# Performance work log

Hardware: AMD Instinct MI355X
Metric: run time of the kernel (lower is better)

The kernel has to match this reference:

```python
import math
import jax, jax.numpy as jnp
import numpy as np

B, N, C = 2, 2048, 1024
H = 16
D = C // H  # 64
LN_EPS = 1e-5


def setup_inputs() -> dict:
    key = jax.random.key(0)
    ks = jax.random.split(key, 5)
    x = jax.random.normal(ks[0], (B, N, C), dtype=jnp.float32)
    w_qkv = jax.random.normal(ks[1], (C, 3 * C), dtype=jnp.float32) * 0.02
    w_proj = jax.random.normal(ks[2], (C, C), dtype=jnp.float32) * 0.02
    b_proj = jnp.zeros((C,), dtype=jnp.float32)
    ln_w = jnp.ones((D,), dtype=jnp.float32) + jax.random.normal(ks[3], (D,), dtype=jnp.float32) * 0.02
    ln_b = jax.random.normal(ks[4], (D,), dtype=jnp.float32) * 0.02
    return {"x": x, "w_qkv": w_qkv, "w_proj": w_proj, "b_proj": b_proj,
            "ln_w": ln_w, "ln_b": ln_b}


def _layernorm(t, w, b):
    mu = jnp.mean(t, axis=-1, keepdims=True)
    var = jnp.var(t, axis=-1, keepdims=True)
    return (t - mu) * jax.lax.rsqrt(var + LN_EPS) * w + b


def reference(x, w_qkv, w_proj, b_proj, ln_w, ln_b):
    b, n, c = x.shape
    h, d = H, c // H
    # QKV projection (no bias): [b,n,3c] -> [3,b,h,n,d]
    qkv = (x @ w_qkv).reshape(b, n, 3, h, d).transpose(2, 0, 3, 1, 4)
    q, k, v = qkv[0], qkv[1], qkv[2]
    # per-head LayerNorm on q and k (qk_norm)
    q = _layernorm(q, ln_w, ln_b)
    k = _layernorm(k, ln_w, ln_b)
    # NOTE: source multiplies q by sqrt(head_dim) (faithful to original)
    q = q * jnp.asarray(math.sqrt(d), dtype=q.dtype)
    scores = jnp.einsum('bhnd,bhmd->bhnm', q, k)  # [b,h,n,n]
    mask_value = -jnp.finfo(scores.dtype).max
    causal = jnp.tril(jnp.ones((n, n), dtype=bool))
    scores = jnp.where(causal, scores, mask_value)
    attn = jax.nn.softmax(scores, axis=-1)
    out = jnp.einsum('bhnm,bhmd->bhnd', attn, v)  # [b,h,n,d]
    out = out.transpose(0, 2, 1, 3).reshape(b, n, c)  # b n (h d)
    return out @ w_proj + b_proj
```

## Files before the change

### kernel.cpp

```cpp
#include <hip/hip_runtime.h>

#define LOG2E 1.4426950408889634f

typedef _Float16 f16x8_t __attribute__((ext_vector_type(8)));
typedef _Float16 f16x4_t __attribute__((ext_vector_type(4)));
typedef _Float16 f16x2_t __attribute__((ext_vector_type(2)));
typedef float    f32x4_t __attribute__((ext_vector_type(4)));

#define MFMA32(a, b, c) __builtin_amdgcn_mfma_f32_16x16x32_f16(a, b, c, 0, 0, 0)
#define MFMA16(a, b, c) __builtin_amdgcn_mfma_f32_16x16x16f16(a, b, c, 0, 0, 0)

__device__ __forceinline__ void async_copy16(void* lds, const void* g) {
    __builtin_amdgcn_global_load_lds(
        (const __attribute__((address_space(1))) unsigned char*)g,
        (__attribute__((address_space(3))) unsigned char*)lds, 16, 0, 0);
}

__global__ void cast_f32_f16_k(const float* __restrict__ in, _Float16* __restrict__ out, int n4) {
    int i = blockIdx.x * blockDim.x + threadIdx.x;
    if (i >= n4) return;
    float4 v = ((const float4*)in)[i];
    f16x4_t o = { (_Float16)v.x, (_Float16)v.y, (_Float16)v.z, (_Float16)v.w };
    ((f16x4_t*)out)[i] = o;
}

__global__ void transpose_cast_k(const float* __restrict__ in, _Float16* __restrict__ out,
                                 int R, int C) {
    __shared__ _Float16 tl[64][65];
    const int t = threadIdx.x;
    const int c = t & 63;
    const int r4 = t >> 6;
    const int r0 = blockIdx.y * 64, c0 = blockIdx.x * 64;
#pragma unroll
    for (int i = 0; i < 16; ++i) {
        int r = r4 + i * 4;
        tl[c][r] = (_Float16)in[(size_t)(r0 + r) * C + c0 + c];
    }
    __syncthreads();
#pragma unroll
    for (int i = 0; i < 16; ++i) {
        int rr = r4 + i * 4;
        out[(size_t)(c0 + rr) * R + r0 + c] = tl[rr][c];
    }
}

__global__ void vtrans_k(const _Float16* __restrict__ qkv, _Float16* __restrict__ VTg) {
    __shared__ _Float16 tl[64][68];
    const int tid = threadIdx.x;
    const int bh = blockIdx.x;
    const int b = bh >> 4, h = bh & 15;
    const int t = blockIdx.y;
    const int c = tid & 63;
    const int r4 = tid >> 6;
#pragma unroll
    for (int i = 0; i < 16; ++i) {
        int r = r4 + i * 4;
        tl[c][r] = qkv[(size_t)(b * 2048 + t * 64 + r) * 3072 + 2048 + h * 64 + c];
    }
    __syncthreads();
    const size_t obase = (size_t)bh * 131072 + (size_t)t * 4096;
#pragma unroll
    for (int e = 0; e < 2; ++e) {
        const int ci = tid * 2 + e;
        const int d = ci >> 3, w = ci & 7;
        const int pq = w ^ (d & 7);
        const int base = (pq >> 2) * 32 + (pq & 3) * 4;
        f16x4_t v0 = *(const f16x4_t*)&tl[d][base];
        f16x4_t v1 = *(const f16x4_t*)&tl[d][base + 16];
        f16x8_t val = __builtin_shufflevector(v0, v1, 0, 1, 2, 3, 4, 5, 6, 7);
        *(f16x8_t*)&VTg[obase + ci * 8] = val;
    }
}

template <typename OutT, bool BIAS>
__global__ __launch_bounds__(256, 3)
void gemm_f16_k(const _Float16* __restrict__ A, const _Float16* __restrict__ BT,
                OutT* __restrict__ C, const float* __restrict__ bias,
                int M, int N, int K) {
    __shared__ _Float16 As[2][128][32];
    __shared__ _Float16 Bs[2][128][32];
    const int tid = threadIdx.x;
    const int wid = tid >> 6, lane = tid & 63;
    const int qd = lane >> 4, ln = lane & 15;
    const int m0 = blockIdx.x * 128, n0 = blockIdx.y * 128;
    const int wm = (wid >> 1) * 64, wn = (wid & 1) * 64;

    f32x4_t acc[4][4] = {};

    const int srow = lane >> 2;
    const int skk  = (lane & 3) * 8;

    for (int k0 = 0; k0 < K; k0 += 64) {
        __syncthreads();
#pragma unroll
        for (int p = 0; p < 4; ++p) {
            const int seg = p * 4 + wid;
            const int s   = seg >> 3;
            const int rg  = seg & 7;
            const int row = rg * 16 + srow;
            const size_t goff = (size_t)row * K + k0 + s * 32 + skk;
            async_copy16(&As[0][0][0] + seg * 512, A  + (size_t)m0 * K + goff);
            async_copy16(&Bs[0][0][0] + seg * 512, BT + (size_t)n0 * K + goff);
        }
        __syncthreads();
#pragma unroll
        for (int s = 0; s < 2; ++s) {
            f16x8_t a[4], b[4];
#pragma unroll
            for (int i = 0; i < 4; ++i)
                a[i] = *(const f16x8_t*)&As[s][wm + i * 16 + ln][qd * 8];
#pragma unroll
            for (int j = 0; j < 4; ++j)
                b[j] = *(const f16x8_t*)&Bs[s][wn + j * 16 + ln][qd * 8];
#pragma unroll
            for (int i = 0; i < 4; ++i)
#pragma unroll
                for (int j = 0; j < 4; ++j)
                    acc[i][j] = MFMA32(a[i], b[j], acc[i][j]);
        }
    }
#pragma unroll
    for (int i = 0; i < 4; ++i)
#pragma unroll
        for (int j = 0; j < 4; ++j) {
            const int col = n0 + wn + j * 16 + ln;
            const float bv = BIAS ? bias[col] : 0.0f;
#pragma unroll
            for (int r = 0; r < 4; ++r) {
                const int row = m0 + wm + i * 16 + qd * 4 + r;
                C[(size_t)row * N + col] = (OutT)(acc[i][j][r] + bv);
            }
        }
}

__global__ __launch_bounds__(256, 2)
void gemm_f16_m64_k(const _Float16* __restrict__ A, const _Float16* __restrict__ BT,
                    float* __restrict__ C, const float* __restrict__ bias,
                    int M, int N, int K) {
    __shared__ _Float16 As[2][64][32];
    __shared__ _Float16 Bs[2][128][32];
    const int tid = threadIdx.x;
    const int wid = tid >> 6, lane = tid & 63;
    const int qd = lane >> 4, ln = lane & 15;
    const int m0 = blockIdx.x * 64, n0 = blockIdx.y * 128;
    const int wn = wid * 32;

    f32x4_t acc[4][2] = {};
    const int srow = lane >> 2;
    const int skk  = (lane & 3) * 8;

    for (int k0 = 0; k0 < K; k0 += 64) {
        __syncthreads();
#pragma unroll
        for (int p = 0; p < 2; ++p) {
            const int seg = p * 4 + wid;
            const int hidx = seg * 512 + lane * 8;
            const int s_ = hidx >> 11;
            const int row = (hidx >> 5) & 63;
            const int kk = hidx & 31;
            async_copy16(&As[0][0][0] + seg * 512,
                         A + (size_t)(m0 + row) * K + k0 + s_ * 32 + kk);
        }
#pragma unroll
        for (int p = 0; p < 4; ++p) {
            const int seg = p * 4 + wid;
            const int s   = seg >> 3;
            const int rg  = seg & 7;
            const int row = rg * 16 + srow;
            async_copy16(&Bs[0][0][0] + seg * 512,
                         BT + (size_t)(n0 + row) * K + k0 + s * 32 + skk);
        }
        __syncthreads();
#pragma unroll
        for (int s = 0; s < 2; ++s) {
            f16x8_t a[4], b[2];
#pragma unroll
            for (int i = 0; i < 4; ++i)
                a[i] = *(const f16x8_t*)&As[s][i * 16 + ln][qd * 8];
#pragma unroll
            for (int j = 0; j < 2; ++j)
                b[j] = *(const f16x8_t*)&Bs[s][wn + j * 16 + ln][qd * 8];
#pragma unroll
            for (int i = 0; i < 4; ++i)
#pragma unroll
                for (int j = 0; j < 2; ++j)
                    acc[i][j] = MFMA32(a[i], b[j], acc[i][j]);
        }
    }
#pragma unroll
    for (int i = 0; i < 4; ++i)
#pragma unroll
        for (int j = 0; j < 2; ++j) {
            const int col = n0 + wn + j * 16 + ln;
            const float bv = bias[col];
#pragma unroll
            for (int r = 0; r < 4; ++r) {
                const int row = m0 + i * 16 + qd * 4 + r;
                C[(size_t)row * N + col] = acc[i][j][r] + bv;
            }
        }
}

__global__ void ln_qk_k(const _Float16* __restrict__ qkv, const float* __restrict__ ln_w,
                        const float* __restrict__ ln_b, _Float16* __restrict__ Qb,
                        _Float16* __restrict__ Kb) {
    const int tid = threadIdx.x;
    const int wid = tid >> 6, lane = tid & 63;
    const int row = blockIdx.x * 4 + wid;
    const int t = row >> 4;
    const int h = row & 15;
    const int b = t >> 11, n = t & 2047;
    const size_t base = (size_t)t * 3072 + h * 64 + lane;
    float q = (float)qkv[base];
    float k = (float)qkv[base + 1024];
    const float wv = ln_w[lane], bv = ln_b[lane];

    float sq = q, sk = k;
#pragma unroll
    for (int m = 1; m < 64; m <<= 1) { sq += __shfl_xor(sq, m); sk += __shfl_xor(sk, m); }
    sq *= (1.0f / 64.0f); sk *= (1.0f / 64.0f);
    const float dq = q - sq, dk = k - sk;
    float vq = dq * dq, vk = dk * dk;
#pragma unroll
    for (int m = 1; m < 64; m <<= 1) { vq += __shfl_xor(vq, m); vk += __shfl_xor(vk, m); }
    vq *= (1.0f / 64.0f); vk *= (1.0f / 64.0f);
    const float yq = dq * rsqrtf(vq + 1e-5f) * wv + bv;
    const float yk = dk * rsqrtf(vk + 1e-5f) * wv + bv;
    const size_t obase = ((size_t)((b * 16 + h) * 2048 + n)) * 64 + lane;
    Qb[obase] = (_Float16)(yq * (8.0f * LOG2E));
    Kb[obase] = (_Float16)yk;
}

__global__ __launch_bounds__(256, 3)
void attn_part_k(const _Float16* __restrict__ Q, const _Float16* __restrict__ K,
                 const _Float16* __restrict__ VTg, _Float16* __restrict__ O,
                 float* __restrict__ Op, float* __restrict__ ml) {
    __shared__ _Float16 Ks[2][2][64][32];
    __shared__ _Float16 VT[2][64][64];

    const int tid = threadIdx.x;
    const int wid = tid >> 6, lane = tid & 63;
    const int qd = lane >> 4, ln = lane & 15;
    const int bh = blockIdx.x;
    const int b = bh >> 4, h = bh & 15;
    const int y = blockIdx.y;
    int band, chunk, nst;
    if (y < 8)       { band = 8 + y;  chunk = 0; nst = 16; }
    else if (y < 16) { band = 23 - y; chunk = 1; nst = 2 * band - 14; }
    else             { band = y - 16; chunk = 0; nst = 2 * band + 2; }
    const size_t kvbase = (size_t)bh * 2048 * 64;
    const size_t vtbase = (size_t)bh * 131072;
    const int qrow0 = band * 128 + wid * 32;
    const int kvbeg = chunk * 1024;

    f16x8_t qf[2][2];
#pragma unroll
    for (int qt = 0; qt < 2; ++qt)
#pragma unroll
        for (int s = 0; s < 2; ++s)
            qf[qt][s] = *(const f16x8_t*)&Q[kvbase + (size_t)(qrow0 + qt * 16 + ln) * 64 + s * 32 + qd * 8];

    f32x4_t o[2][4] = {};
    f32x4_t ls[2] = {};
    float m[2] = { -3.0e38f, -3.0e38f };
    const f16x4_t ones = { (_Float16)1.0f, (_Float16)1.0f, (_Float16)1.0f, (_Float16)1.0f };

    auto stage = [&](int buf, int kv0) {
#pragma unroll
        for (int p = 0; p < 2; ++p) {
            const int seg = p * 4 + wid;
            const int hidx = seg * 512 + lane * 8;
            const int s_ = hidx >> 11;
            const int rrow = (hidx >> 5) & 63;
            const int kk = hidx & 31;
            async_copy16(&Ks[buf][0][0][0] + seg * 512,
                         K + kvbase + (size_t)(kv0 + rrow) * 64 + s_ * 32 + kk);
        }
#pragma unroll
        for (int p = 0; p < 2; ++p) {
            const int seg = p * 4 + wid;
            async_copy16(&VT[buf][0][0] + seg * 512,
                         VTg + vtbase + (size_t)kv0 * 64 + seg * 512 + lane * 8);
        }
    };

    stage(0, kvbeg);

    for (int st = 0; st < nst; ++st) {
        const int kv0 = kvbeg + st * 64;
        __syncthreads();
        if (st + 1 < nst) stage((st + 1) & 1, kv0 + 64);
        const int buf = st & 1;

        if (kv0 <= qrow0 + 31) {
            f32x4_t sc[2][4];
#pragma unroll
            for (int jt = 0; jt < 4; ++jt) {
                f16x8_t k0 = *(const f16x8_t*)&Ks[buf][0][jt * 16 + ln][qd * 8];
                f16x8_t k1 = *(const f16x8_t*)&Ks[buf][1][jt * 16 + ln][qd * 8];
#pragma unroll
                for (int qt = 0; qt < 2; ++qt) {
                    f32x4_t s = {};
                    s = MFMA32(k0, qf[qt][0], s);
                    s = MFMA32(k1, qf[qt][1], s);
                    sc[qt][jt] = s;
                }
            }
            f16x8_t vf8[4][2];
#pragma unroll
            for (int dt = 0; dt < 4; ++dt)
#pragma unroll
                for (int pp = 0; pp < 2; ++pp) {
                    const int w = (pp * 4 + qd) ^ (ln & 7);
                    vf8[dt][pp] = *(const f16x8_t*)&VT[buf][dt * 16 + ln][w * 8];
                }

#pragma unroll
            for (int qt = 0; qt < 2; ++qt) {
                if (kv0 + 63 > qrow0 + qt * 16) {
                    const int qq = qrow0 + qt * 16 + ln;
#pragma unroll
                    for (int c = 0; c < 4; ++c)
#pragma unroll
                        for (int r = 0; r < 4; ++r)
                            if (kv0 + c * 16 + qd * 4 + r > qq) sc[qt][c][r] = -3.0e38f;
                }
                f32x4_t mq = sc[qt][0];
#pragma unroll
                for (int c = 1; c < 4; ++c)
#pragma unroll
                    for (int r = 0; r < 4; ++r) mq[r] = fmaxf(mq[r], sc[qt][c][r]);
                float mx = fmaxf(fmaxf(mq[0], mq[1]), fmaxf(mq[2], mq[3]));
                mx = fmaxf(mx, __shfl_xor(mx, 16));
                mx = fmaxf(mx, __shfl_xor(mx, 32));
                if (!__all(mx <= m[qt] + 8.0f)) {
                    const float mn = fmaxf(m[qt], mx);
                    const float al = exp2f(m[qt] - mn);
#pragma unroll
                    for (int dt = 0; dt < 4; ++dt) o[qt][dt] *= al;
                    ls[qt][0] *= al;
                    m[qt] = mn;
                }
                f16x4_t pf[4];
#pragma unroll
                for (int c = 0; c < 4; ++c) {
                    float p0 = exp2f(sc[qt][c][0] - m[qt]);
                    float p1 = exp2f(sc[qt][c][1] - m[qt]);
                    float p2 = exp2f(sc[qt][c][2] - m[qt]);
                    float p3 = exp2f(sc[qt][c][3] - m[qt]);
                    f16x2_t a = __builtin_bit_cast(f16x2_t, __builtin_amdgcn_cvt_pkrtz(p0, p1));
                    f16x2_t bb = __builtin_bit_cast(f16x2_t, __builtin_amdgcn_cvt_pkrtz(p2, p3));
                    pf[c] = __builtin_shufflevector(a, bb, 0, 1, 2, 3);
                }
#pragma unroll
                for (int c = 0; c < 4; ++c) ls[qt] = MFMA16(ones, pf[c], ls[qt]);
#pragma unroll
                for (int dt = 0; dt < 4; ++dt)
#pragma unroll
                    for (int pp = 0; pp < 2; ++pp) {
                        f16x4_t lo = __builtin_shufflevector(vf8[dt][pp], vf8[dt][pp], 0, 1, 2, 3);
                        f16x4_t hi = __builtin_shufflevector(vf8[dt][pp], vf8[dt][pp], 4, 5, 6, 7);
                        o[qt][dt] = MFMA16(lo, pf[pp * 2 + 0], o[qt][dt]);
                        o[qt][dt] = MFMA16(hi, pf[pp * 2 + 1], o[qt][dt]);
                    }
            }
        }
    }

    if (band < 8) {
        const size_t base0 = ((size_t)(b * 2048 + qrow0 + ln)) * 1024 + h * 64 + qd * 4;
#pragma unroll
        for (int qt = 0; qt < 2; ++qt) {
            const float inv = 1.0f / ls[qt][0];
            const size_t base = base0 + (size_t)qt * 16 * 1024;
#pragma unroll
            for (int dt = 0; dt < 4; ++dt) {
                f16x4_t ov;
#pragma unroll
                for (int r = 0; r < 4; ++r) ov[r] = (_Float16)(o[qt][dt][r] * inv);
                *(f16x4_t*)&O[base + dt * 16] = ov;
            }
        }
    } else {
        const size_t pb = ((size_t)bh * 8 + (band - 8)) * 2 + chunk;
#pragma unroll
        for (int qt = 0; qt < 2; ++qt) {
            const int row = wid * 32 + qt * 16 + ln;
            float* op = Op + pb * 8192 + (size_t)row * 64 + qd * 4;
#pragma unroll
            for (int dt = 0; dt < 4; ++dt)
                *(f32x4_t*)&op[dt * 16] = o[qt][dt];
            if (qd == 0) {
                ml[pb * 256 + row * 2]     = m[qt];
                ml[pb * 256 + row * 2 + 1] = ls[qt][0];
            }
        }
    }
}

__global__ __launch_bounds__(256)
void attn_merge_k(const float* __restrict__ Op, const float* __restrict__ ml,
                  _Float16* __restrict__ O) {
    const int bh = blockIdx.x, bnd = blockIdx.y;
    const int b = bh >> 4, h = bh & 15;
    const int band = 8 + bnd;
    const size_t pb = ((size_t)bh * 8 + bnd) * 2;
    const int tid = threadIdx.x;
    const int row = tid >> 1;
    const int c32 = (tid & 1) * 32;
    const float m0 = ml[pb * 256 + row * 2],       l0 = ml[pb * 256 + row * 2 + 1];
    const float m1 = ml[(pb + 1) * 256 + row * 2], l1 = ml[(pb + 1) * 256 + row * 2 + 1];
    const float mm = fmaxf(m0, m1);
    const float a0 = exp2f(m0 - mm), a1 = exp2f(m1 - mm);
    const float inv = 1.0f / (l0 * a0 + l1 * a1);
    const float* p0 = Op + pb * 8192 + (size_t)row * 64 + c32;
    const float* p1 = p0 + 8192;
    _Float16* op = O + ((size_t)(b * 2048 + band * 128 + row)) * 1024 + h * 64 + c32;
#pragma unroll
    for (int g = 0; g < 8; ++g) {
        f32x4_t v0 = *(const f32x4_t*)&p0[g * 4];
        f32x4_t v1 = *(const f32x4_t*)&p1[g * 4];
        f16x4_t ov;
#pragma unroll
        for (int r = 0; r < 4; ++r)
            ov[r] = (_Float16)((v0[r] * a0 + v1[r] * a1) * inv);
        *(f16x4_t*)&op[g * 4] = ov;
    }
}

extern "C" void kernel_launch(void* const* d_in, const int* in_sizes, int n_in,
                              void* d_out, int out_size, void* d_ws, size_t ws_size,
                              hipStream_t stream) {
    const float* x      = (const float*)d_in[0];
    const float* w_qkv  = (const float*)d_in[1];
    const float* w_proj = (const float*)d_in[2];
    const float* b_proj = (const float*)d_in[3];
    const float* ln_w   = (const float*)d_in[4];
    const float* ln_b   = (const float*)d_in[5];
    float* out = (float*)d_out;

    char* w = (char*)d_ws;
    _Float16*  qkv    = (_Float16*)w;  w += (size_t)4096 * 3072 * 2;
    _Float16*  xh     = (_Float16*)w;  w += (size_t)4096 * 1024 * 2;
    _Float16*  wqkvT  = (_Float16*)w;  w += (size_t)3072 * 1024 * 2;
    _Float16*  wprojT = (_Float16*)w;  w += (size_t)1024 * 1024 * 2;
    _Float16*  Qb     = (_Float16*)w;  w += (size_t)32 * 2048 * 64 * 2;
    _Float16*  Kb     = (_Float16*)w;  w += (size_t)32 * 2048 * 64 * 2;
    _Float16*  VTg    = (_Float16*)w;  w += (size_t)32 * 64 * 2048 * 2;
    _Float16*  Ah     = (_Float16*)w;  w += (size_t)4096 * 1024 * 2;
    float*     Op     = (float*)w;     w += (size_t)32 * 8 * 2 * 8192 * 4;
    float*     mlb    = (float*)w;     w += (size_t)32 * 8 * 2 * 256 * 4;

    cast_f32_f16_k<<<4096, 256, 0, stream>>>(x, xh, 4096 * 1024 / 4);
    transpose_cast_k<<<dim3(48, 16), 256, 0, stream>>>(w_qkv, wqkvT, 1024, 3072);
    transpose_cast_k<<<dim3(16, 16), 256, 0, stream>>>(w_proj, wprojT, 1024, 1024);
    gemm_f16_k<_Float16, false><<<dim3(32, 24), 256, 0, stream>>>(xh, wqkvT, qkv, nullptr, 4096, 3072, 1024);
    vtrans_k<<<dim3(32, 32), 256, 0, stream>>>(qkv, VTg);
    ln_qk_k<<<16384, 256, 0, stream>>>(qkv, ln_w, ln_b, Qb, Kb);
    attn_part_k<<<dim3(32, 24), 256, 0, stream>>>(Qb, Kb, VTg, Ah, Op, mlb);
    attn_merge_k<<<dim3(32, 8), 256, 0, stream>>>(Op, mlb, Ah);
    gemm_f16_m64_k<<<dim3(64, 8), 256, 0, stream>>>(Ah, wprojT, out, b_proj, 4096, 1024, 1024);
}
```

Baseline: 213.6 us.

## Split causal attention into 512-key chunks across 40 blocks per head

New measurement: 300.7 us. 40.8% more time.

```diff
diff --git a/kernel.cpp b/kernel.cpp
--- a/kernel.cpp
+++ b/kernel.cpp
@@ -231,7 +231,7 @@
     Kb[obase] = (_Float16)yk;
 }
 
-__global__ __launch_bounds__(256, 3)
+__global__ __launch_bounds__(256, 4)
 void attn_part_k(const _Float16* __restrict__ Q, const _Float16* __restrict__ K,
                  const _Float16* __restrict__ VTg, _Float16* __restrict__ O,
                  float* __restrict__ Op, float* __restrict__ ml) {
@@ -244,14 +244,17 @@
     const int bh = blockIdx.x;
     const int b = bh >> 4, h = bh & 15;
     const int y = blockIdx.y;
-    int band, chunk, nst;
-    if (y < 8)       { band = 8 + y;  chunk = 0; nst = 16; }
-    else if (y < 16) { band = 23 - y; chunk = 1; nst = 2 * band - 14; }
-    else             { band = y - 16; chunk = 0; nst = 2 * band + 2; }
+    int g, j;
+    if (y < 16)      { g = y;      j = 0; }
+    else if (y < 28) { g = y - 12; j = 1; }
+    else if (y < 36) { g = y - 20; j = 2; }
+    else             { g = y - 24; j = 3; }
+    const int beg = j * 8;
+    const int nst = min(2 * g + 2, beg + 8) - beg;
     const size_t kvbase = (size_t)bh * 2048 * 64;
     const size_t vtbase = (size_t)bh * 131072;
-    const int qrow0 = band * 128 + wid * 32;
-    const int kvbeg = chunk * 1024;
+    const int qrow0 = g * 128 + wid * 32;
+    const int kvbeg = j * 512;
 
     f16x8_t qf[2][2];
 #pragma unroll
@@ -352,6 +355,7 @@
                     f16x2_t bb = __builtin_bit_cast(f16x2_t, __builtin_amdgcn_cvt_pkrtz(p2, p3));
                     pf[c] = __builtin_shufflevector(a, bb, 0, 1, 2, 3);
                 }
+                __builtin_amdgcn_s_setprio(1);
 #pragma unroll
                 for (int c = 0; c < 4; ++c) ls[qt] = MFMA16(ones, pf[c], ls[qt]);
 #pragma unroll
@@ -363,11 +367,12 @@
                         o[qt][dt] = MFMA16(lo, pf[pp * 2 + 0], o[qt][dt]);
                         o[qt][dt] = MFMA16(hi, pf[pp * 2 + 1], o[qt][dt]);
                     }
-            }
-        }
-    }
-
-    if (band < 8) {
+                __builtin_amdgcn_s_setprio(0);
+            }
+        }
+    }
+
+    if (g < 4) {
         const size_t base0 = ((size_t)(b * 2048 + qrow0 + ln)) * 1024 + h * 64 + qd * 4;
 #pragma unroll
         for (int qt = 0; qt < 2; ++qt) {
@@ -382,7 +387,8 @@
             }
         }
     } else {
-        const size_t pb = ((size_t)bh * 8 + (band - 8)) * 2 + chunk;
+        const int off = (g < 8) ? (g - 4) * 2 : (g < 12) ? 8 + (g - 8) * 3 : 20 + (g - 12) * 4;
+        const size_t pb = (size_t)bh * 36 + off + j;
 #pragma unroll
         for (int qt = 0; qt < 2; ++qt) {
             const int row = wid * 32 + qt * 16 + ln;
@@ -401,30 +407,50 @@
 __global__ __launch_bounds__(256)
 void attn_merge_k(const float* __restrict__ Op, const float* __restrict__ ml,
                   _Float16* __restrict__ O) {
-    const int bh = blockIdx.x, bnd = blockIdx.y;
+    const int bh = blockIdx.x;
+    const int g = 4 + blockIdx.y;
     const int b = bh >> 4, h = bh & 15;
-    const int band = 8 + bnd;
-    const size_t pb = ((size_t)bh * 8 + bnd) * 2;
+    const int nu = ((2 * g + 1) >> 3) + 1;
+    const int off = (g < 8) ? (g - 4) * 2 : (g < 12) ? 8 + (g - 8) * 3 : 20 + (g - 12) * 4;
+    const size_t pb0 = (size_t)bh * 36 + off;
     const int tid = threadIdx.x;
     const int row = tid >> 1;
     const int c32 = (tid & 1) * 32;
-    const float m0 = ml[pb * 256 + row * 2],       l0 = ml[pb * 256 + row * 2 + 1];
-    const float m1 = ml[(pb + 1) * 256 + row * 2], l1 = ml[(pb + 1) * 256 + row * 2 + 1];
-    const float mm = fmaxf(m0, m1);
-    const float a0 = exp2f(m0 - mm), a1 = exp2f(m1 - mm);
-    const float inv = 1.0f / (l0 * a0 + l1 * a1);
-    const float* p0 = Op + pb * 8192 + (size_t)row * 64 + c32;
-    const float* p1 = p0 + 8192;
-    _Float16* op = O + ((size_t)(b * 2048 + band * 128 + row)) * 1024 + h * 64 + c32;
-#pragma unroll
-    for (int g = 0; g < 8; ++g) {
-        f32x4_t v0 = *(const f32x4_t*)&p0[g * 4];
-        f32x4_t v1 = *(const f32x4_t*)&p1[g * 4];
+
+    float mj[4], lj[4], aj[4];
+    float mm = -3.0e38f;
+#pragma unroll
+    for (int u = 0; u < 4; ++u)
+        if (u < nu) {
+            mj[u] = ml[(pb0 + u) * 256 + row * 2];
+            lj[u] = ml[(pb0 + u) * 256 + row * 2 + 1];
+            mm = fmaxf(mm, mj[u]);
+        }
+    float lsum = 0.0f;
+#pragma unroll
+    for (int u = 0; u < 4; ++u)
+        if (u < nu) {
+            aj[u] = exp2f(mj[u] - mm);
+            lsum += lj[u] * aj[u];
+        }
+    const float inv = 1.0f / lsum;
+
+    _Float16* op = O + ((size_t)(b * 2048 + g * 128 + row)) * 1024 + h * 64 + c32;
+#pragma unroll
+    for (int seg = 0; seg < 8; ++seg) {
+        f32x4_t acc = {};
+#pragma unroll
+        for (int u = 0; u < 4; ++u)
+            if (u < nu) {
+                const float* p = Op + (pb0 + u) * 8192 + (size_t)row * 64 + c32;
+                f32x4_t v = *(const f32x4_t*)&p[seg * 4];
+#pragma unroll
+                for (int r = 0; r < 4; ++r) acc[r] += v[r] * aj[u];
+            }
         f16x4_t ov;
 #pragma unroll
-        for (int r = 0; r < 4; ++r)
-            ov[r] = (_Float16)((v0[r] * a0 + v1[r] * a1) * inv);
-        *(f16x4_t*)&op[g * 4] = ov;
+        for (int r = 0; r < 4; ++r) ov[r] = (_Float16)(acc[r] * inv);
+        *(f16x4_t*)&op[seg * 4] = ov;
     }
 }
 
@@ -440,16 +466,17 @@
     float* out = (float*)d_out;
 
     char* w = (char*)d_ws;
-    _Float16*  qkv    = (_Float16*)w;  w += (size_t)4096 * 3072 * 2;
-    _Float16*  xh     = (_Float16*)w;  w += (size_t)4096 * 1024 * 2;
-    _Float16*  wqkvT  = (_Float16*)w;  w += (size_t)3072 * 1024 * 2;
-    _Float16*  wprojT = (_Float16*)w;  w += (size_t)1024 * 1024 * 2;
-    _Float16*  Qb     = (_Float16*)w;  w += (size_t)32 * 2048 * 64 * 2;
-    _Float16*  Kb     = (_Float16*)w;  w += (size_t)32 * 2048 * 64 * 2;
-    _Float16*  VTg    = (_Float16*)w;  w += (size_t)32 * 64 * 2048 * 2;
-    _Float16*  Ah     = (_Float16*)w;  w += (size_t)4096 * 1024 * 2;
-    float*     Op     = (float*)w;     w += (size_t)32 * 8 * 2 * 8192 * 4;
-    float*     mlb    = (float*)w;     w += (size_t)32 * 8 * 2 * 256 * 4;
+    const size_t MB = 1024 * 1024;
+    _Float16*  qkv    = (_Float16*)(w);
+    _Float16*  xh     = (_Float16*)(w + 24 * MB);
+    _Float16*  wqkvT  = (_Float16*)(w + 32 * MB);
+    _Float16*  wprojT = (_Float16*)(w + 38 * MB);
+    _Float16*  Qb     = (_Float16*)(w + 40 * MB);
+    _Float16*  Kb     = (_Float16*)(w + 48 * MB);
+    _Float16*  VTg    = (_Float16*)(w + 56 * MB);
+    _Float16*  Ah     = (_Float16*)(w + 64 * MB);
+    float*     Op     = (float*)(w);
+    float*     mlb    = (float*)(w + 36 * MB);
 
     cast_f32_f16_k<<<4096, 256, 0, stream>>>(x, xh, 4096 * 1024 / 4);
     transpose_cast_k<<<dim3(48, 16), 256, 0, stream>>>(w_qkv, wqkvT, 1024, 3072);
@@ -457,7 +484,7 @@
     gemm_f16_k<_Float16, false><<<dim3(32, 24), 256, 0, stream>>>(xh, wqkvT, qkv, nullptr, 4096, 3072, 1024);
     vtrans_k<<<dim3(32, 32), 256, 0, stream>>>(qkv, VTg);
     ln_qk_k<<<16384, 256, 0, stream>>>(qkv, ln_w, ln_b, Qb, Kb);
-    attn_part_k<<<dim3(32, 24), 256, 0, stream>>>(Qb, Kb, VTg, Ah, Op, mlb);
-    attn_merge_k<<<dim3(32, 8), 256, 0, stream>>>(Op, mlb, Ah);
+    attn_part_k<<<dim3(32, 40), 256, 0, stream>>>(Qb, Kb, VTg, Ah, Op, mlb);
+    attn_merge_k<<<dim3(32, 12), 256, 0, stream>>>(Op, mlb, Ah);
     gemm_f16_m64_k<<<dim3(64, 8), 256, 0, stream>>>(Ah, wprojT, out, b_proj, 4096, 1024, 1024);
 }
```

## Fuse QK layernorm into QKV GEMM epilogue and merge prep kernels

Applied to the files above, without the earlier changes.

Result: faster. 194.0 us (-9.2%).

```diff
diff --git a/kernel.cpp b/kernel.cpp
--- a/kernel.cpp
+++ b/kernel.cpp
@@ -16,21 +16,25 @@
         (__attribute__((address_space(3))) unsigned char*)lds, 16, 0, 0);
 }
 
-__global__ void cast_f32_f16_k(const float* __restrict__ in, _Float16* __restrict__ out, int n4) {
-    int i = blockIdx.x * blockDim.x + threadIdx.x;
-    if (i >= n4) return;
-    float4 v = ((const float4*)in)[i];
-    f16x4_t o = { (_Float16)v.x, (_Float16)v.y, (_Float16)v.z, (_Float16)v.w };
-    ((f16x4_t*)out)[i] = o;
-}
-
-__global__ void transpose_cast_k(const float* __restrict__ in, _Float16* __restrict__ out,
-                                 int R, int C) {
+__global__ void prep_k(const float* __restrict__ x, _Float16* __restrict__ xh,
+                       const float* __restrict__ wq, _Float16* __restrict__ wqT,
+                       const float* __restrict__ wp, _Float16* __restrict__ wpT) {
     __shared__ _Float16 tl[64][65];
-    const int t = threadIdx.x;
+    const int bx = blockIdx.x, t = threadIdx.x;
+    if (bx < 4096) {
+        const int i = bx * 256 + t;
+        float4 v = ((const float4*)x)[i];
+        f16x4_t o = { (_Float16)v.x, (_Float16)v.y, (_Float16)v.z, (_Float16)v.w };
+        ((f16x4_t*)xh)[i] = o;
+        return;
+    }
+    const float* in; _Float16* out; int C, bxx, byy;
+    if (bx < 4864) { const int id = bx - 4096; in = wq; out = wqT; C = 3072; bxx = id % 48; byy = id / 48; }
+    else           { const int id = bx - 4864; in = wp; out = wpT; C = 1024; bxx = id % 16; byy = id / 16; }
+    const int R = 1024;
     const int c = t & 63;
     const int r4 = t >> 6;
-    const int r0 = blockIdx.y * 64, c0 = blockIdx.x * 64;
+    const int r0 = byy * 64, c0 = bxx * 64;
 #pragma unroll
     for (int i = 0; i < 16; ++i) {
         int r = r4 + i * 4;
@@ -72,10 +76,11 @@
     }
 }
 
-template <typename OutT, bool BIAS>
+template <typename OutT, bool BIAS, bool LNQK>
 __global__ __launch_bounds__(256, 3)
 void gemm_f16_k(const _Float16* __restrict__ A, const _Float16* __restrict__ BT,
                 OutT* __restrict__ C, const float* __restrict__ bias,
+                const float* __restrict__ ln_w, const float* __restrict__ ln_b,
                 int M, int N, int K) {
     __shared__ _Float16 As[2][128][32];
     __shared__ _Float16 Bs[2][128][32];
@@ -119,6 +124,35 @@
                     acc[i][j] = MFMA32(a[i], b[j], acc[i][j]);
         }
     }
+
+    if constexpr (LNQK) {
+        if (n0 < 2048) {
+            const float scale = (n0 < 1024) ? 8.0f * LOG2E : 1.0f;
+            float lw[4], lb[4];
+#pragma unroll
+            for (int j = 0; j < 4; ++j) { lw[j] = ln_w[j * 16 + ln]; lb[j] = ln_b[j * 16 + ln]; }
+#pragma unroll
+            for (int i = 0; i < 4; ++i)
+#pragma unroll
+                for (int r = 0; r < 4; ++r) {
+                    float s = acc[i][0][r] + acc[i][1][r] + acc[i][2][r] + acc[i][3][r];
+                    s += __shfl_xor(s, 1); s += __shfl_xor(s, 2);
+                    s += __shfl_xor(s, 4); s += __shfl_xor(s, 8);
+                    const float mu = s * 0.015625f;
+                    const float d0 = acc[i][0][r] - mu, d1 = acc[i][1][r] - mu;
+                    const float d2 = acc[i][2][r] - mu, d3 = acc[i][3][r] - mu;
+                    float v = d0 * d0 + d1 * d1 + d2 * d2 + d3 * d3;
+                    v += __shfl_xor(v, 1); v += __shfl_xor(v, 2);
+                    v += __shfl_xor(v, 4); v += __shfl_xor(v, 8);
+                    const float rs = rsqrtf(v * 0.015625f + 1e-5f);
+                    acc[i][0][r] = (d0 * rs * lw[0] + lb[0]) * scale;
+                    acc[i][1][r] = (d1 * rs * lw[1] + lb[1]) * scale;
+                    acc[i][2][r] = (d2 * rs * lw[2] + lb[2]) * scale;
+                    acc[i][3][r] = (d3 * rs * lw[3] + lb[3]) * scale;
+                }
+        }
+    }
+
 #pragma unroll
     for (int i = 0; i < 4; ++i)
 #pragma unroll
@@ -201,40 +235,9 @@
         }
 }
 
-__global__ void ln_qk_k(const _Float16* __restrict__ qkv, const float* __restrict__ ln_w,
-                        const float* __restrict__ ln_b, _Float16* __restrict__ Qb,
-                        _Float16* __restrict__ Kb) {
-    const int tid = threadIdx.x;
-    const int wid = tid >> 6, lane = tid & 63;
-    const int row = blockIdx.x * 4 + wid;
-    const int t = row >> 4;
-    const int h = row & 15;
-    const int b = t >> 11, n = t & 2047;
-    const size_t base = (size_t)t * 3072 + h * 64 + lane;
-    float q = (float)qkv[base];
-    float k = (float)qkv[base + 1024];
-    const float wv = ln_w[lane], bv = ln_b[lane];
-
-    float sq = q, sk = k;
-#pragma unroll
-    for (int m = 1; m < 64; m <<= 1) { sq += __shfl_xor(sq, m); sk += __shfl_xor(sk, m); }
-    sq *= (1.0f / 64.0f); sk *= (1.0f / 64.0f);
-    const float dq = q - sq, dk = k - sk;
-    float vq = dq * dq, vk = dk * dk;
-#pragma unroll
-    for (int m = 1; m < 64; m <<= 1) { vq += __shfl_xor(vq, m); vk += __shfl_xor(vk, m); }
-    vq *= (1.0f / 64.0f); vk *= (1.0f / 64.0f);
-    const float yq = dq * rsqrtf(vq + 1e-5f) * wv + bv;
-    const float yk = dk * rsqrtf(vk + 1e-5f) * wv + bv;
-    const size_t obase = ((size_t)((b * 16 + h) * 2048 + n)) * 64 + lane;
-    Qb[obase] = (_Float16)(yq * (8.0f * LOG2E));
-    Kb[obase] = (_Float16)yk;
-}
-
 __global__ __launch_bounds__(256, 3)
-void attn_part_k(const _Float16* __restrict__ Q, const _Float16* __restrict__ K,
-                 const _Float16* __restrict__ VTg, _Float16* __restrict__ O,
-                 float* __restrict__ Op, float* __restrict__ ml) {
+void attn_part_k(const _Float16* __restrict__ qkv, const _Float16* __restrict__ VTg,
+                 _Float16* __restrict__ O, float* __restrict__ Op, float* __restrict__ ml) {
     __shared__ _Float16 Ks[2][2][64][32];
     __shared__ _Float16 VT[2][64][64];
 
@@ -248,7 +251,6 @@
     if (y < 8)       { band = 8 + y;  chunk = 0; nst = 16; }
     else if (y < 16) { band = 23 - y; chunk = 1; nst = 2 * band - 14; }
     else             { band = y - 16; chunk = 0; nst = 2 * band + 2; }
-    const size_t kvbase = (size_t)bh * 2048 * 64;
     const size_t vtbase = (size_t)bh * 131072;
     const int qrow0 = band * 128 + wid * 32;
     const int kvbeg = chunk * 1024;
@@ -258,7 +260,8 @@
     for (int qt = 0; qt < 2; ++qt)
 #pragma unroll
         for (int s = 0; s < 2; ++s)
-            qf[qt][s] = *(const f16x8_t*)&Q[kvbase + (size_t)(qrow0 + qt * 16 + ln) * 64 + s * 32 + qd * 8];
+            qf[qt][s] = *(const f16x8_t*)&qkv[(size_t)(b * 2048 + qrow0 + qt * 16 + ln) * 3072
+                                             + h * 64 + s * 32 + qd * 8];
 
     f32x4_t o[2][4] = {};
     f32x4_t ls[2] = {};
@@ -274,7 +277,8 @@
             const int rrow = (hidx >> 5) & 63;
             const int kk = hidx & 31;
             async_copy16(&Ks[buf][0][0][0] + seg * 512,
-                         K + kvbase + (size_t)(kv0 + rrow) * 64 + s_ * 32 + kk);
+                         qkv + (size_t)(b * 2048 + kv0 + rrow) * 3072 + 1024 + h * 64
+                             + s_ * 32 + kk);
         }
 #pragma unroll
         for (int p = 0; p < 2; ++p) {
@@ -352,6 +356,7 @@
                     f16x2_t bb = __builtin_bit_cast(f16x2_t, __builtin_amdgcn_cvt_pkrtz(p2, p3));
                     pf[c] = __builtin_shufflevector(a, bb, 0, 1, 2, 3);
                 }
+                __builtin_amdgcn_s_setprio(1);
 #pragma unroll
                 for (int c = 0; c < 4; ++c) ls[qt] = MFMA16(ones, pf[c], ls[qt]);
 #pragma unroll
@@ -363,6 +368,7 @@
                         o[qt][dt] = MFMA16(lo, pf[pp * 2 + 0], o[qt][dt]);
                         o[qt][dt] = MFMA16(hi, pf[pp * 2 + 1], o[qt][dt]);
                     }
+                __builtin_amdgcn_s_setprio(0);
             }
         }
     }
@@ -440,24 +446,21 @@
     float* out = (float*)d_out;
 
     char* w = (char*)d_ws;
-    _Float16*  qkv    = (_Float16*)w;  w += (size_t)4096 * 3072 * 2;
-    _Float16*  xh     = (_Float16*)w;  w += (size_t)4096 * 1024 * 2;
-    _Float16*  wqkvT  = (_Float16*)w;  w += (size_t)3072 * 1024 * 2;
-    _Float16*  wprojT = (_Float16*)w;  w += (size_t)1024 * 1024 * 2;
-    _Float16*  Qb     = (_Float16*)w;  w += (size_t)32 * 2048 * 64 * 2;
-    _Float16*  Kb     = (_Float16*)w;  w += (size_t)32 * 2048 * 64 * 2;
-    _Float16*  VTg    = (_Float16*)w;  w += (size_t)32 * 64 * 2048 * 2;
-    _Float16*  Ah     = (_Float16*)w;  w += (size_t)4096 * 1024 * 2;
-    float*     Op     = (float*)w;     w += (size_t)32 * 8 * 2 * 8192 * 4;
-    float*     mlb    = (float*)w;     w += (size_t)32 * 8 * 2 * 256 * 4;
-
-    cast_f32_f16_k<<<4096, 256, 0, stream>>>(x, xh, 4096 * 1024 / 4);
-    transpose_cast_k<<<dim3(48, 16), 256, 0, stream>>>(w_qkv, wqkvT, 1024, 3072);
-    transpose_cast_k<<<dim3(16, 16), 256, 0, stream>>>(w_proj, wprojT, 1024, 1024);
-    gemm_f16_k<_Float16, false><<<dim3(32, 24), 256, 0, stream>>>(xh, wqkvT, qkv, nullptr, 4096, 3072, 1024);
+    const size_t MB = 1024 * 1024;
+    _Float16*  qkv    = (_Float16*)(w);
+    _Float16*  xh     = (_Float16*)(w + 24 * MB);
+    _Float16*  wqkvT  = (_Float16*)(w + 32 * MB);
+    _Float16*  wprojT = (_Float16*)(w + 38 * MB);
+    _Float16*  VTg    = (_Float16*)(w + 40 * MB);
+    _Float16*  Ah     = (_Float16*)(w + 48 * MB);
+    float*     Op     = (float*)(w + 56 * MB);
+    float*     mlb    = (float*)(w + 72 * MB);
+
+    prep_k<<<5120, 256, 0, stream>>>(x, xh, w_qkv, wqkvT, w_proj, wprojT);
+    gemm_f16_k<_Float16, false, true><<<dim3(32, 24), 256, 0, stream>>>(
+        xh, wqkvT, qkv, nullptr, ln_w, ln_b, 4096, 3072, 1024);
     vtrans_k<<<dim3(32, 32), 256, 0, stream>>>(qkv, VTg);
-    ln_qk_k<<<16384, 256, 0, stream>>>(qkv, ln_w, ln_b, Qb, Kb);
-    attn_part_k<<<dim3(32, 24), 256, 0, stream>>>(Qb, Kb, VTg, Ah, Op, mlb);
+    attn_part_k<<<dim3(32, 24), 256, 0, stream>>>(qkv, VTg, Ah, Op, mlb);
     attn_merge_k<<<dim3(32, 8), 256, 0, stream>>>(Op, mlb, Ah);
     gemm_f16_m64_k<<<dim3(64, 8), 256, 0, stream>>>(Ah, wprojT, out, b_proj, 4096, 1024, 1024);
 }
```
